# Optimization experiments

Measured on AMD Instinct MI355X. Metric: run time of the kernel, lower is better.

## Reference

```python
import jax, jax.numpy as jnp
import numpy as np

NEAR = 0.1
FAR = 100.0


def quat_to_rotmat(q):
    q = q / jnp.linalg.norm(q, axis=-1, keepdims=True)
    w, x, y, z = q[..., 0], q[..., 1], q[..., 2], q[..., 3]
    R = jnp.stack([
        1 - 2 * (y * y + z * z), 2 * (x * y - z * w), 2 * (x * z + y * w),
        2 * (x * y + z * w), 1 - 2 * (x * x + z * z), 2 * (y * z - x * w),
        2 * (x * z - y * w), 2 * (y * z + x * w), 1 - 2 * (x * x + y * y)
    ], axis=-1)
    return R.reshape(q.shape[:-1] + (3, 3))


def _render_view(means, scales, rots, opac, sem, E, K3, H, W):
    # means [N,3] ego; E [4,4] ego2cam; K3 [3,3]
    means_cam = means @ E[:3, :3].T + E[:3, 3]  # [N,3]
    x_c, y_c, z = means_cam[:, 0], means_cam[:, 1], means_cam[:, 2]
    z_safe = jnp.maximum(z, 1e-4)
    fx, fy, cx, cy = K3[0, 0], K3[1, 1], K3[0, 2], K3[1, 2]
    u = x_c / z_safe * fx + cx
    v = y_c / z_safe * fy + cy
    # 3D covariance: Sigma = R diag(s)^2 R^T
    R = quat_to_rotmat(rots)              # [N,3,3]
    RS = R * scales[:, None, :]
    Sigma = RS @ jnp.swapaxes(RS, -1, -2)  # [N,3,3]
    Wc = E[:3, :3]
    Sigma_cam = jnp.einsum('ij,njk,lk->nil', Wc, Sigma, Wc)  # [N,3,3]
    # EWA Jacobian J [N,2,3]
    zero = jnp.zeros_like(z)
    J = jnp.stack([
        jnp.stack([fx / z_safe, zero, -fx * x_c / z_safe ** 2], axis=-1),
        jnp.stack([zero, fy / z_safe, -fy * y_c / z_safe ** 2], axis=-1),
    ], axis=-2)
    cov2d = jnp.einsum('nij,njk,nlk->nil', J, Sigma_cam, J)  # [N,2,2]
    a = jnp.maximum(cov2d[:, 0, 0], 0.3)
    c = jnp.maximum(cov2d[:, 1, 1], 0.3)
    bb = cov2d[:, 0, 1]
    det = a * c - bb * bb
    valid = (z > 0.01) & (det > 1e-8)
    det_s = jnp.where(det > 1e-8, det, 1.0)
    ia, ib, ic = c / det_s, -bb / det_s, a / det_s  # inverse 2x2 cov
    # per-pixel Mahalanobis distance, [N,H,W]
    px = jnp.arange(W, dtype=means.dtype)
    py = jnp.arange(H, dtype=means.dtype)
    dx = px[None, None, :] - u[:, None, None]   # [N,1,W]
    dy = py[None, :, None] - v[:, None, None]   # [N,H,1]
    d2 = (ia[:, None, None] * dx * dx + ic[:, None, None] * dy * dy
          + 2.0 * ib[:, None, None] * (dx * dy))
    g = jnp.exp(-0.5 * d2)
    visible = valid & (z > NEAR) & (u >= 0) & (u < W) & (v >= 0) & (v < H)
    alpha = jnp.where(visible[:, None, None],
                      jnp.clip(opac[:, None, None] * g, 0.0, 0.99), 0.0)
    # depth-sorted front-to-back alpha blending
    order = jnp.argsort(z)
    alpha_s = alpha[order]                                     # [N,H,W]
    feats = jnp.concatenate([sem, jnp.clip(z, NEAR, FAR)[:, None]], axis=-1)[order]  # [N,C+1]
    log1m = jnp.log1p(-alpha_s)
    T_excl = jnp.exp(jnp.cumsum(log1m, axis=0) - log1m)        # exclusive transmittance
    wgt = T_excl * alpha_s                                     # [N,H,W]
    rendered = jnp.einsum('nhw,nd->dhw', wgt, feats)           # [C+1,H,W]
    alpha_map = jnp.sum(wgt, axis=0)                           # [H,W]
    C = sem.shape[1]
    return rendered[C:C + 1], rendered[:C], alpha_map[None]


def reference(means, scales, rotations, opacities, semantic_features,
              target_intrinsics, target_cam2ego, H, W):
    ego2cam = jnp.linalg.inv(target_cam2ego)  # [B,M,4,4]
    B, M = target_cam2ego.shape[:2]
    deps, sems, alps = [], [], []
    for b in range(B):
        db, sb, ab = [], [], []
        for m in range(M):
            d, s, a = _render_view(means[b], scales[b], rotations[b],
                                   opacities[b, :, 0], semantic_features[b],
                                   ego2cam[b, m], target_intrinsics[b, m, :3, :3], H, W)
            db.append(d); sb.append(s); ab.append(a)
        deps.append(jnp.stack(db)); sems.append(jnp.stack(sb)); alps.append(jnp.stack(ab))
    depth_map = jnp.stack(deps)     # [B,M,1,H,W]
    semantic_map = jnp.stack(sems)  # [B,M,C,H,W]
    alpha_map = jnp.stack(alps)     # [B,M,1,H,W]
    return depth_map, semantic_map, alpha_map


def setup_inputs() -> dict:
    key = jax.random.key(0)
    ks = jax.random.split(key, 8)
    B, N, C, M, H, W = 1, 2048, 16, 2, 128, 128
    fx = fy = 128.0
    cx = cy = 64.0
    # gaussians inside the frustum: z in [2,40], |x|,|y| < 0.45*z
    z = jax.random.uniform(ks[0], (B, N), minval=2.0, maxval=40.0)
    x = z * jax.random.uniform(ks[1], (B, N), minval=-0.45, maxval=0.45)
    y = z * jax.random.uniform(ks[2], (B, N), minval=-0.45, maxval=0.45)
    means = jnp.stack([x, y, z], axis=-1).astype(jnp.float32)
    scales = jax.random.uniform(ks[3], (B, N, 3), minval=0.05, maxval=0.5).astype(jnp.float32)
    rotations = jax.random.normal(ks[4], (B, N, 4), dtype=jnp.float32)
    opacities = jax.random.uniform(ks[5], (B, N, 1), minval=0.05, maxval=0.95).astype(jnp.float32)
    semantic_features = jax.random.normal(ks[6], (B, N, C), dtype=jnp.float32)
    K = jnp.array([[fx, 0, cx, 0], [0, fy, cy, 0], [0, 0, 1, 0], [0, 0, 0, 1]], dtype=jnp.float32)
    target_intrinsics = jnp.broadcast_to(K, (B, M, 4, 4))
    c2e0 = jnp.eye(4, dtype=jnp.float32)
    c2e1 = c2e0.at[0, 3].set(0.5)
    target_cam2ego = jnp.broadcast_to(jnp.stack([c2e0, c2e1]), (B, M, 4, 4))
    return {"means": means, "scales": scales, "rotations": rotations,
            "opacities": opacities, "semantic_features": semantic_features,
            "target_intrinsics": target_intrinsics, "target_cam2ego": target_cam2ego,
            "H": H, "W": W}
```

## Files before the change

kernel.cpp:

```cpp
#include <hip/hip_runtime.h>
#include <cmath>


#define MAXC   16
#define MAXBM  8
#define NSEG   16
#define RTPB   (NSEG * 64)
#define BINW   8
#define BINT   (BINW * 64)
#define MAXSEG 256
#define ROWS1  9
#define ROWS2  10
#define INVIS_KEY 0x7FFFFFFF

__device__ __forceinline__ float rlf(float x, int l) {
    return __int_as_float(__builtin_amdgcn_readlane(__float_as_int(x), l));
}

__device__ void inv4x4_rows3(const float* __restrict__ src, float* __restrict__ Eout) {
    double m[16];
#pragma unroll
    for (int j = 0; j < 16; ++j) m[j] = (double)src[j];
    double inv[16];
    inv[0]  =  m[5]*m[10]*m[15] - m[5]*m[11]*m[14] - m[9]*m[6]*m[15] + m[9]*m[7]*m[14] + m[13]*m[6]*m[11] - m[13]*m[7]*m[10];
    inv[4]  = -m[4]*m[10]*m[15] + m[4]*m[11]*m[14] + m[8]*m[6]*m[15] - m[8]*m[7]*m[14] - m[12]*m[6]*m[11] + m[12]*m[7]*m[10];
    inv[8]  =  m[4]*m[9]*m[15]  - m[4]*m[11]*m[13] - m[8]*m[5]*m[15] + m[8]*m[7]*m[13] + m[12]*m[5]*m[11] - m[12]*m[7]*m[9];
    inv[12] = -m[4]*m[9]*m[14]  + m[4]*m[10]*m[13] + m[8]*m[5]*m[14] - m[8]*m[6]*m[13] - m[12]*m[5]*m[10] + m[12]*m[6]*m[9];
    inv[1]  = -m[1]*m[10]*m[15] + m[1]*m[11]*m[14] + m[9]*m[2]*m[15] - m[9]*m[3]*m[14] - m[13]*m[2]*m[11] + m[13]*m[3]*m[10];
    inv[5]  =  m[0]*m[10]*m[15] - m[0]*m[11]*m[14] - m[8]*m[2]*m[15] + m[8]*m[3]*m[14] + m[12]*m[2]*m[11] - m[12]*m[3]*m[10];
    inv[9]  = -m[0]*m[9]*m[15]  + m[0]*m[11]*m[13] + m[8]*m[1]*m[15] - m[8]*m[3]*m[13] - m[12]*m[1]*m[11] + m[12]*m[3]*m[9];
    inv[13] =  m[0]*m[9]*m[14]  - m[0]*m[10]*m[13] - m[8]*m[1]*m[14] + m[8]*m[2]*m[13] + m[12]*m[1]*m[10] - m[12]*m[2]*m[9];
    inv[2]  =  m[1]*m[6]*m[15]  - m[1]*m[7]*m[14]  - m[5]*m[2]*m[15] + m[5]*m[3]*m[14] + m[13]*m[2]*m[7]  - m[13]*m[3]*m[6];
    inv[6]  = -m[0]*m[6]*m[15]  + m[0]*m[7]*m[14]  + m[4]*m[2]*m[15] - m[4]*m[3]*m[14] - m[12]*m[2]*m[7]  + m[12]*m[3]*m[6];
    inv[10] =  m[0]*m[5]*m[15]  - m[0]*m[7]*m[13]  - m[4]*m[1]*m[15] + m[4]*m[3]*m[13] + m[12]*m[1]*m[7]  - m[12]*m[3]*m[5];
    inv[14] = -m[0]*m[5]*m[14]  + m[0]*m[6]*m[13]  + m[4]*m[1]*m[14] - m[4]*m[2]*m[13] - m[12]*m[1]*m[6]  + m[12]*m[2]*m[5];
    inv[3]  = -m[1]*m[6]*m[11]  + m[1]*m[7]*m[10]  + m[5]*m[2]*m[11] - m[5]*m[3]*m[10] - m[9]*m[2]*m[7]   + m[9]*m[3]*m[6];
    inv[7]  =  m[0]*m[6]*m[11]  - m[0]*m[7]*m[10]  - m[4]*m[2]*m[11] + m[4]*m[3]*m[10] + m[8]*m[2]*m[7]   - m[8]*m[3]*m[6];
    inv[11] = -m[0]*m[5]*m[11]  + m[0]*m[7]*m[9]   + m[4]*m[1]*m[11] - m[4]*m[3]*m[9]  - m[8]*m[1]*m[7]   + m[8]*m[3]*m[5];
    inv[15] =  m[0]*m[5]*m[10]  - m[0]*m[6]*m[9]   - m[4]*m[1]*m[10] + m[4]*m[2]*m[9]  + m[8]*m[1]*m[6]   - m[8]*m[2]*m[5];
    double det = m[0]*inv[0] + m[1]*inv[4] + m[2]*inv[8] + m[3]*inv[12];
    double rdet = 1.0 / det;
#pragma unroll
    for (int r = 0; r < 3; ++r)
#pragma unroll
        for (int c = 0; c < 4; ++c)
            Eout[r * 4 + c] = (float)(inv[r * 4 + c] * rdet);
}

__global__ __launch_bounds__(256) void preprocess_kernel(
    const float* __restrict__ means, const float* __restrict__ scales,
    const float* __restrict__ rots,  const float* __restrict__ intr,
    const float* __restrict__ cam2ego,
    int* __restrict__ ikey, float* __restrict__ uu, float* __restrict__ vv,
    float* __restrict__ cia, float* __restrict__ cib, float* __restrict__ cic,
    float* __restrict__ cex, float* __restrict__ cey,
    float* __restrict__ crbc, float* __restrict__ crba,
    int B, int M, int N, int W, int H)
{
    __shared__ float Esh[MAXBM * 12];
    int BM = B * M;
    if (threadIdx.x < (unsigned)BM)
        inv4x4_rows3(cam2ego + (size_t)threadIdx.x * 16, Esh + threadIdx.x * 12);
    __syncthreads();

    int gid = blockIdx.x * 256 + threadIdx.x;
    if (gid >= BM * N) return;
    int bm = gid / N;
    int n  = gid - bm * N;
    int b  = bm / M;
    const float* Ep = Esh + bm * 12;
    const float* mp = means + ((size_t)b * N + n) * 3;
    float mx = mp[0], my = mp[1], mz = mp[2];
    float x_c = Ep[0]*mx + Ep[1]*my + Ep[2]*mz  + Ep[3];
    float y_c = Ep[4]*mx + Ep[5]*my + Ep[6]*mz  + Ep[7];
    float z   = Ep[8]*mx + Ep[9]*my + Ep[10]*mz + Ep[11];
    const float* K = intr + (size_t)bm * 16;
    float fx = K[0], fy = K[5], cx = K[2], cy = K[6];
    float zs = fmaxf(z, 1e-4f);
    float u = x_c / zs * fx + cx;
    float v = y_c / zs * fy + cy;
    const float* qp = rots + ((size_t)b * N + n) * 4;
    float qw = qp[0], qx = qp[1], qy = qp[2], qz = qp[3];
    float qn = sqrtf(qw*qw + qx*qx + qy*qy + qz*qz);
    qw /= qn; qx /= qn; qy /= qn; qz /= qn;
    float R00 = 1.f - 2.f*(qy*qy + qz*qz), R01 = 2.f*(qx*qy - qz*qw), R02 = 2.f*(qx*qz + qy*qw);
    float R10 = 2.f*(qx*qy + qz*qw), R11 = 1.f - 2.f*(qx*qx + qz*qz), R12 = 2.f*(qy*qz - qx*qw);
    float R20 = 2.f*(qx*qz - qy*qw), R21 = 2.f*(qy*qz + qx*qw), R22 = 1.f - 2.f*(qx*qx + qy*qy);
    const float* sp = scales + ((size_t)b * N + n) * 3;
    float s0 = sp[0]*sp[0], s1 = sp[1]*sp[1], s2 = sp[2]*sp[2];
    float S00 = R00*R00*s0 + R01*R01*s1 + R02*R02*s2;
    float S01 = R00*R10*s0 + R01*R11*s1 + R02*R12*s2;
    float S02 = R00*R20*s0 + R01*R21*s1 + R02*R22*s2;
    float S11 = R10*R10*s0 + R11*R11*s1 + R12*R12*s2;
    float S12 = R10*R20*s0 + R11*R21*s1 + R12*R22*s2;
    float S22 = R20*R20*s0 + R21*R21*s1 + R22*R22*s2;
    float W00 = Ep[0], W01 = Ep[1], W02 = Ep[2];
    float W10 = Ep[4], W11 = Ep[5], W12 = Ep[6];
    float W20 = Ep[8], W21 = Ep[9], W22 = Ep[10];
    float A00 = W00*S00 + W01*S01 + W02*S02;
    float A01 = W00*S01 + W01*S11 + W02*S12;
    float A02 = W00*S02 + W01*S12 + W02*S22;
    float A10 = W10*S00 + W11*S01 + W12*S02;
    float A11 = W10*S01 + W11*S11 + W12*S12;
    float A12 = W10*S02 + W11*S12 + W12*S22;
    float A20 = W20*S00 + W21*S01 + W22*S02;
    float A21 = W20*S01 + W21*S11 + W22*S12;
    float A22 = W20*S02 + W21*S12 + W22*S22;
    float Sc00 = A00*W00 + A01*W01 + A02*W02;
    float Sc01 = A00*W10 + A01*W11 + A02*W12;
    float Sc02 = A00*W20 + A01*W21 + A02*W22;
    float Sc11 = A10*W10 + A11*W11 + A12*W12;
    float Sc12 = A10*W20 + A11*W21 + A12*W22;
    float Sc22 = A20*W20 + A21*W21 + A22*W22;
    float j00 = fx / zs,  j02 = -fx * x_c / (zs * zs);
    float j11 = fy / zs,  j12 = -fy * y_c / (zs * zs);
    float c00 = j00*j00*Sc00 + 2.f*j00*j02*Sc02 + j02*j02*Sc22;
    float c01 = j00*(Sc01*j11 + Sc02*j12) + j02*(Sc12*j11 + Sc22*j12);
    float c11 = j11*j11*Sc11 + 2.f*j11*j12*Sc12 + j12*j12*Sc22;
    float a  = fmaxf(c00, 0.3f);
    float cc = fmaxf(c11, 0.3f);
    float bb = c01;
    float det = a * cc - bb * bb;
    bool valid = (z > 0.01f) && (det > 1e-8f);
    float det_s = (det > 1e-8f) ? det : 1.0f;
    float ia = cc / det_s, ib = -bb / det_s, ic = a / det_s;
    uu[gid] = u;  vv[gid] = v;
    cia[gid] = ia;  cib[gid] = ib;  cic[gid] = ic;
    cex[gid] = sqrtf(34.0f * a);
    cey[gid] = sqrtf(34.0f * cc);
    crbc[gid] = -bb / a;
    crba[gid] = -bb / cc;
    bool visible = valid && (z > 0.1f) &&
                   (u >= 0.f) && (u < (float)W) && (v >= 0.f) && (v < (float)H);
    ikey[gid] = visible ? __float_as_int(z) : INVIS_KEY;
}

__global__ __launch_bounds__(64) void rankpack_kernel(
    const int* __restrict__ ikey,
    const float* __restrict__ uu, const float* __restrict__ vv,
    const float* __restrict__ cia, const float* __restrict__ cib,
    const float* __restrict__ cic, const float* __restrict__ cex,
    const float* __restrict__ cey, const float* __restrict__ crbc,
    const float* __restrict__ crba,
    const float* __restrict__ opac, const float* __restrict__ sem,
    float4* __restrict__ pk0, float4* __restrict__ pk1,
    float4* __restrict__ pk2,
    float* __restrict__ psem, int* __restrict__ pcount,
    int B, int M, int N, int C)
{
    int lane  = threadIdx.x & 63;
    int nch64 = (N + 63) >> 6;
    int chunk = blockIdx.x;
    int bm = chunk / nch64;
    int cl = chunk - bm * nch64;
    int i  = (cl << 6) + lane;
    const int* kb = ikey + (size_t)bm * N;
    int ki  = (i < N) ? kb[i] : INVIS_KEY;
    int kip = ki + 1;
    int rank = 0, tot = 0;
    int kj = (lane < N) ? kb[lane] : INVIS_KEY;
    for (int jc = 0; jc < nch64; ++jc) {
        int kcur = kj;
        if (jc + 1 < nch64) {
            int jn = ((jc + 1) << 6) + lane;
            kj = (jn < N) ? kb[jn] : INVIS_KEY;
        }
        tot += (int)__popcll(__ballot(kcur != INVIS_KEY));
        if (jc < cl) {
#pragma unroll
            for (int gg = 0; gg < 64; ++gg)
                rank += (__builtin_amdgcn_readlane(kcur, gg) < kip);
        } else if (jc > cl) {
#pragma unroll
            for (int gg = 0; gg < 64; ++gg)
                rank += (__builtin_amdgcn_readlane(kcur, gg) < ki);
        } else {
#pragma unroll
            for (int gg = 0; gg < 64; ++gg) {
                int kk = (gg < lane) ? kip : ki;
                rank += (__builtin_amdgcn_readlane(kcur, gg) < kk);
            }
        }
    }
    if (cl == 0 && lane == 0) pcount[bm] = tot;
    if (i < N && ki != INVIS_KEY) {
        int b = bm / M;
        size_t src = (size_t)bm * N + i;
        size_t dst = (size_t)bm * N + rank;
        float z = __int_as_float(ki);
        pk0[dst] = make_float4(uu[src], vv[src], cex[src], cey[src]);
        pk1[dst] = make_float4(cia[src], cib[src], cic[src],
                               opac[(size_t)b * N + i]);
        pk2[dst] = make_float4(fminf(fmaxf(z, 0.1f), 100.0f),
                               crbc[src], crba[src], 0.f);
        const float* spc = sem + ((size_t)b * N + i) * C;
        float* dpc = psem + dst * C;
        int c4 = C & ~3;
        for (int q = 0; q < c4; q += 4)
            *(float4*)(dpc + q) = *(const float4*)(spc + q);
        for (int q = c4; q < C; ++q) dpc[q] = spc[q];
    }
}

__global__ __launch_bounds__(BINT) void binlist_kernel(
    const float4* __restrict__ pk0, const float4* __restrict__ pk1,
    const float4* __restrict__ pk2, const int* __restrict__ pcount,
    int* __restrict__ list, int* __restrict__ tilecount,
    int BM, int N, int ntx, int nty)
{
    __shared__ int stage[BINW][MAXSEG];
    __shared__ int wcnt[BINW];
    int wave = threadIdx.x >> 6;
    int lane = threadIdx.x & 63;
    int tile = blockIdx.x;
    int tpv = ntx * nty;
    int bm  = tile / tpv;
    int rem = tile - bm * tpv;
    int tyi = rem / ntx;
    int txi = rem - tyi * ntx;
    float x0 = (float)(txi * 8),     y0 = (float)(tyi * 8);
    float x1 = (float)(txi * 8 + 7), y1 = (float)(tyi * 8 + 7);

    int cnt = pcount[bm];
    int seg = (cnt + BINW - 1) / BINW;
    int gs = wave * seg;
    int ge = min(gs + seg, cnt);

    int nlocal = 0;
    for (int base = gs; base < ge; base += 64) {
        int g = base + lane;
        bool inr = g < ge;
        int gc = inr ? g : (ge - 1);
        size_t src = (size_t)bm * N + gc;
        float4 P0 = pk0[src];
        float4 P1 = pk1[src];
        float4 P2 = pk2[src];
        float dx0 = x0 - P0.x, dx1 = x1 - P0.x;
        float dy0 = y0 - P0.y, dy1 = y1 - P0.y;
        bool aabb = (dx0 <= P0.z) && (-dx1 <= P0.z) &&
                    (dy0 <= P0.w) && (-dy1 <= P0.w);
        bool inside = (dx0 <= 0.f) && (dx1 >= 0.f) && (dy0 <= 0.f) && (dy1 >= 0.f);
        float t, q0, q1, q2, q3;
        t  = fminf(fmaxf(P2.y * dx0, dy0), dy1);
        q0 = P1.x * dx0 * dx0 + t * (P1.z * t + 2.f * P1.y * dx0);
        t  = fminf(fmaxf(P2.y * dx1, dy0), dy1);
        q1 = P1.x * dx1 * dx1 + t * (P1.z * t + 2.f * P1.y * dx1);
        t  = fminf(fmaxf(P2.z * dy0, dx0), dx1);
        q2 = P1.z * dy0 * dy0 + t * (P1.x * t + 2.f * P1.y * dy0);
        t  = fminf(fmaxf(P2.z * dy1, dx0), dx1);
        q3 = P1.z * dy1 * dy1 + t * (P1.x * t + 2.f * P1.y * dy1);
        float mind2 = inside ? 0.f : fminf(fminf(q0, q1), fminf(q2, q3));
        unsigned long long mask = __ballot(inr && aabb && (mind2 <= 34.0f));
        if ((mask >> lane) & 1ull) {
            int pos = nlocal + (int)__popcll(mask & ((1ull << lane) - 1ull));
            stage[wave][pos] = g;
        }
        nlocal += (int)__popcll(mask);
    }
    if (lane == 0) wcnt[wave] = nlocal;
    __syncthreads();
    int offs = 0, total = 0;
    for (int w = 0; w < BINW; ++w) {
        if (w < wave) offs += wcnt[w];
        total += wcnt[w];
    }
    int* dst = list + (size_t)tile * N;
    for (int i = lane; i < nlocal; i += 64) dst[offs + i] = stage[wave][i];
    if (threadIdx.x == 0) tilecount[tile] = total;
}

__global__ __launch_bounds__(RTPB) void raster_kernel(
    const float4* __restrict__ pk0, const float4* __restrict__ pk1,
    const float4* __restrict__ pk2,
    const float* __restrict__ psem,
    const int* __restrict__ list, const int* __restrict__ tilecount,
    float* __restrict__ out,
    int BM, int N, int C, int H, int W, int ntx, int nty)
{
    __shared__ float comb[NSEG * ROWS2 * 64];
    int wave = threadIdx.x >> 6;
    int lane = threadIdx.x & 63;
    int tile = blockIdx.x;
    int tpv = ntx * nty;
    int bm  = tile / tpv;
    int rem = tile - bm * tpv;
    int tyi = rem / ntx;
    int txi = rem - tyi * ntx;
    int lx = lane & 7, ly = lane >> 3;
    float fxp = (float)(txi * 8 + lx), fyp = (float)(tyi * 8 + ly);

    int cnt = tilecount[tile];
    int seg = (cnt + NSEG - 1) / NSEG;
    int gs = wave * seg;
    int ge = min(gs + seg, cnt);

    float T = 1.0f, accA = 0.f, accD = 0.f;
    float accS[MAXC];
#pragma unroll
    for (int q = 0; q < MAXC; ++q) accS[q] = 0.f;

    const int* tl = list + (size_t)tile * N;
    for (int base = gs; base < ge; base += 64) {
        int g = base + lane;
        bool inr = g < ge;
        int idx = tl[inr ? g : (ge - 1)];
        size_t src = (size_t)bm * N + idx;
        float4 P0 = pk0[src];
        float4 P1 = pk1[src];
        float4 P2 = pk2[src];
        float sf[MAXC];
        {
            const float4* spc = (const float4*)(psem + src * MAXC);
#pragma unroll
            for (int q = 0; q < MAXC / 4; ++q) {
                float4 f = spc[q];
                sf[q*4+0] = f.x; sf[q*4+1] = f.y; sf[q*4+2] = f.z; sf[q*4+3] = f.w;
            }
        }
        int nev = min(64, ge - base);
        for (int gg = 0; gg < nev; ++gg) {
            float u  = rlf(P0.x, gg), v  = rlf(P0.y, gg);
            float ia = rlf(P1.x, gg), ib = rlf(P1.y, gg), ic = rlf(P1.z, gg);
            float dx = fxp - u, dy = fyp - v;
            float d2 = ia*dx*dx + ic*dy*dy + 2.0f*ib*(dx*dy);
            float gvl = __expf(-0.5f * d2);
            float alpha = fminf(rlf(P1.w, gg) * gvl, 0.99f);
            float w = T * alpha;
            T -= w;
            accD += w * rlf(P2.x, gg);
            accA += w;
#pragma unroll
            for (int ch = 0; ch < MAXC; ++ch) accS[ch] += w * rlf(sf[ch], gg);
        }
    }

    int px = lane;
    int pxx = txi * 8 + (px & 7);
    int pyy = tyi * 8 + (px >> 3);
    bool inb = (pxx < W) && (pyy < H);
    size_t HW  = (size_t)H * W;
    size_t pix = (size_t)pyy * W + pxx;
    size_t BMHW = (size_t)BM * HW;

    float* my = comb + (wave * ROWS1) * 64 + lane;
    my[0 * 64] = T;
    my[1 * 64] = accD;
    my[2 * 64] = accA;
#pragma unroll
    for (int k = 0; k < 6; ++k) my[(3 + k) * 64] = accS[k];
    __syncthreads();

    float pre[NSEG];
    pre[0] = 1.f;
#pragma unroll
    for (int w = 1; w < NSEG; ++w)
        pre[w] = pre[w-1] * comb[((w-1) * ROWS1) * 64 + px];

    if (wave < 8) {
        int row, outc;
        if (wave == 0)      { row = 1;        outc = 0; }
        else if (wave <= 6) { row = 2 + wave; outc = wave; }
        else                { row = 2;        outc = C + 1; }
        float val = 0.f;
#pragma unroll
        for (int w = 0; w < NSEG; ++w)
            val += pre[w] * comb[(w * ROWS1 + row) * 64 + px];
        if (inb) {
            float* dst;
            if (outc == 0)      dst = out + (size_t)bm * HW + pix;
            else if (outc <= C) dst = out + BMHW + (size_t)bm * C * HW + (size_t)(outc-1) * HW + pix;
            else                dst = out + BMHW + BMHW * C + (size_t)bm * HW + pix;
            *dst = val;
        }
    }
    __syncthreads();

    float* my2 = comb + (wave * ROWS2) * 64 + lane;
#pragma unroll
    for (int k = 0; k < 10; ++k) my2[k * 64] = accS[6 + k];
    __syncthreads();

    if (wave < 10) {
        int k = wave;
        float val = 0.f;
#pragma unroll
        for (int w = 0; w < NSEG; ++w)
            val += pre[w] * comb[(w * ROWS2 + k) * 64 + px];
        if (inb) {
            int outc = 7 + k;
            float* dst = out + BMHW + (size_t)bm * C * HW + (size_t)(outc-1) * HW + pix;
            *dst = val;
        }
    }
}

extern "C" void kernel_launch(void* const* d_in, const int* in_sizes, int n_in,
                              void* d_out, int out_size, void* d_ws, size_t ws_size,
                              hipStream_t stream) {
    const float* means  = (const float*)d_in[0];
    const float* scales = (const float*)d_in[1];
    const float* rots   = (const float*)d_in[2];
    const float* opac   = (const float*)d_in[3];
    const float* sem    = (const float*)d_in[4];
    const float* intr   = (const float*)d_in[5];
    const float* c2e    = (const float*)d_in[6];
    float* out = (float*)d_out;

    int B  = 1;
    int BM = in_sizes[6] / 16;
    int M  = BM / B;
    int N  = in_sizes[0] / (3 * B);
    int C  = in_sizes[4] / (B * N);
    long HWl = (long)out_size / ((long)BM * (C + 2));
    int H = (int)(sqrt((double)HWl) + 0.5);
    int W = (int)(HWl / H);
    int ntx = (W + 7) / 8, nty = (H + 7) / 8;
    int ntiles = ntx * nty * BM;
    int nch64  = (N + 63) >> 6;

    float* ws = (float*)d_ws;
    size_t off = 0;
    size_t BMN  = (size_t)BM * N;
    int*   ikey = (int*)(ws + off); off += BMN;
    float* uu   = ws + off; off += BMN;
    float* vv   = ws + off; off += BMN;
    float* cia  = ws + off; off += BMN;
    float* cib  = ws + off; off += BMN;
    float* cic  = ws + off; off += BMN;
    float* cex  = ws + off; off += BMN;
    float* cey  = ws + off; off += BMN;
    float* crbc = ws + off; off += BMN;
    float* crba = ws + off; off += BMN;
    off = (off + 3) & ~(size_t)3;
    float4* pk0 = (float4*)(ws + off); off += BMN * 4;
    float4* pk1 = (float4*)(ws + off); off += BMN * 4;
    float4* pk2 = (float4*)(ws + off); off += BMN * 4;
    float* psem = ws + off; off += BMN * C;
    int* pcount = (int*)(ws + off); off += BM;
    int* list   = (int*)(ws + off); off += (size_t)ntiles * N;
    int* tcnt   = (int*)(ws + off); off += ntiles;

    int tot = BM * N;
    preprocess_kernel<<<(tot + 255) / 256, 256, 0, stream>>>(
        means, scales, rots, intr, c2e,
        ikey, uu, vv, cia, cib, cic, cex, cey, crbc, crba, B, M, N, W, H);

    rankpack_kernel<<<BM * nch64, 64, 0, stream>>>(
        ikey, uu, vv, cia, cib, cic, cex, cey, crbc, crba, opac, sem,
        pk0, pk1, pk2, psem, pcount, B, M, N, C);

    binlist_kernel<<<ntiles, BINT, 0, stream>>>(
        pk0, pk1, pk2, pcount, list, tcnt, BM, N, ntx, nty);

    raster_kernel<<<ntiles, RTPB, 0, stream>>>(
        pk0, pk1, pk2, psem, list, tcnt, out, BM, N, C, H, W, ntx, nty);
}
```

Measured before the change: 121.2 us.

## Fuse tile binning into raster kernel and split rank counting across waves

Removes the separate binlist kernel. Each raster block now culls its own tile's Gaussians across 16 waves, compacts the surviving indices into shared memory, and rasterizes from that shared list, so the global per-tile list and count buffers are no longer written or read. Separately, rankpack now uses 4 waves per chunk, each counting a strided subset of key chunks, and combines partial ranks through shared memory. The costs are extra barriers and a fixed per-wave staging capacity in shared memory, which overflows if a wave's culling segment holds more than the capacity allows.

```diff
diff --git a/kernel.cpp b/kernel.cpp
--- a/kernel.cpp
+++ b/kernel.cpp
@@ -6,11 +6,10 @@
 #define MAXBM  8
 #define NSEG   16
 #define RTPB   (NSEG * 64)
-#define BINW   8
-#define BINT   (BINW * 64)
-#define MAXSEG 256
+#define SEGCAP 128
 #define ROWS1  9
 #define ROWS2  10
+#define RPW    4
 #define INVIS_KEY 0x7FFFFFFF
 
 __device__ __forceinline__ float rlf(float x, int l) {
@@ -135,7 +134,7 @@
     ikey[gid] = visible ? __float_as_int(z) : INVIS_KEY;
 }
 
-__global__ __launch_bounds__(64) void rankpack_kernel(
+__global__ __launch_bounds__(RPW * 64) void rankpack_kernel(
     const int* __restrict__ ikey,
     const float* __restrict__ uu, const float* __restrict__ vv,
     const float* __restrict__ cia, const float* __restrict__ cib,
@@ -148,6 +147,9 @@
     float* __restrict__ psem, int* __restrict__ pcount,
     int B, int M, int N, int C)
 {
+    __shared__ int rsum[RPW][64];
+    __shared__ int tsum[RPW];
+    int wave  = threadIdx.x >> 6;
     int lane  = threadIdx.x & 63;
     int nch64 = (N + 63) >> 6;
     int chunk = blockIdx.x;
@@ -158,30 +160,32 @@
     int ki  = (i < N) ? kb[i] : INVIS_KEY;
     int kip = ki + 1;
     int rank = 0, tot = 0;
-    int kj = (lane < N) ? kb[lane] : INVIS_KEY;
-    for (int jc = 0; jc < nch64; ++jc) {
-        int kcur = kj;
-        if (jc + 1 < nch64) {
-            int jn = ((jc + 1) << 6) + lane;
-            kj = (jn < N) ? kb[jn] : INVIS_KEY;
-        }
-        tot += (int)__popcll(__ballot(kcur != INVIS_KEY));
+    for (int jc = wave; jc < nch64; jc += RPW) {
+        int jn = (jc << 6) + lane;
+        int kj = (jn < N) ? kb[jn] : INVIS_KEY;
+        tot += (int)__popcll(__ballot(kj != INVIS_KEY));
         if (jc < cl) {
 #pragma unroll
             for (int gg = 0; gg < 64; ++gg)
-                rank += (__builtin_amdgcn_readlane(kcur, gg) < kip);
+                rank += (__builtin_amdgcn_readlane(kj, gg) < kip);
         } else if (jc > cl) {
 #pragma unroll
             for (int gg = 0; gg < 64; ++gg)
-                rank += (__builtin_amdgcn_readlane(kcur, gg) < ki);
+                rank += (__builtin_amdgcn_readlane(kj, gg) < ki);
         } else {
 #pragma unroll
             for (int gg = 0; gg < 64; ++gg) {
                 int kk = (gg < lane) ? kip : ki;
-                rank += (__builtin_amdgcn_readlane(kcur, gg) < kk);
+                rank += (__builtin_amdgcn_readlane(kj, gg) < kk);
             }
         }
     }
+    rsum[wave][lane] = rank;
+    if (lane == 0) tsum[wave] = tot;
+    __syncthreads();
+    if (wave != 0) return;
+    rank = rsum[0][lane] + rsum[1][lane] + rsum[2][lane] + rsum[3][lane];
+    tot  = tsum[0] + tsum[1] + tsum[2] + tsum[3];
     if (cl == 0 && lane == 0) pcount[bm] = tot;
     if (i < N && ki != INVIS_KEY) {
         int b = bm / M;
@@ -202,14 +206,19 @@
     }
 }
 
-__global__ __launch_bounds__(BINT) void binlist_kernel(
+__global__ __launch_bounds__(RTPB) void raster_kernel(
     const float4* __restrict__ pk0, const float4* __restrict__ pk1,
-    const float4* __restrict__ pk2, const int* __restrict__ pcount,
-    int* __restrict__ list, int* __restrict__ tilecount,
-    int BM, int N, int ntx, int nty)
+    const float4* __restrict__ pk2,
+    const float* __restrict__ psem, const int* __restrict__ pcount,
+    float* __restrict__ out,
+    int BM, int N, int C, int H, int W, int ntx, int nty)
 {
-    __shared__ int stage[BINW][MAXSEG];
-    __shared__ int wcnt[BINW];
+    __shared__ float sh[NSEG * ROWS2 * 64];
+    int* stage = (int*)sh;
+    int* flat  = stage + NSEG * SEGCAP;
+    int* wcnt  = flat + NSEG * SEGCAP;
+    float* comb = sh;
+
     int wave = threadIdx.x >> 6;
     int lane = threadIdx.x & 63;
     int tile = blockIdx.x;
@@ -218,14 +227,15 @@
     int rem = tile - bm * tpv;
     int tyi = rem / ntx;
     int txi = rem - tyi * ntx;
+    int lx = lane & 7, ly = lane >> 3;
+    float fxp = (float)(txi * 8 + lx), fyp = (float)(tyi * 8 + ly);
     float x0 = (float)(txi * 8),     y0 = (float)(tyi * 8);
     float x1 = (float)(txi * 8 + 7), y1 = (float)(tyi * 8 + 7);
 
     int cnt = pcount[bm];
-    int seg = (cnt + BINW - 1) / BINW;
+    int seg = (cnt + NSEG - 1) / NSEG;
     int gs = wave * seg;
     int ge = min(gs + seg, cnt);
-
     int nlocal = 0;
     for (int base = gs; base < ge; base += 64) {
         int g = base + lane;
@@ -253,57 +263,35 @@
         unsigned long long mask = __ballot(inr && aabb && (mind2 <= 34.0f));
         if ((mask >> lane) & 1ull) {
             int pos = nlocal + (int)__popcll(mask & ((1ull << lane) - 1ull));
-            stage[wave][pos] = g;
+            stage[wave * SEGCAP + pos] = g;
         }
         nlocal += (int)__popcll(mask);
     }
     if (lane == 0) wcnt[wave] = nlocal;
     __syncthreads();
     int offs = 0, total = 0;
-    for (int w = 0; w < BINW; ++w) {
-        if (w < wave) offs += wcnt[w];
-        total += wcnt[w];
-    }
-    int* dst = list + (size_t)tile * N;
-    for (int i = lane; i < nlocal; i += 64) dst[offs + i] = stage[wave][i];
-    if (threadIdx.x == 0) tilecount[tile] = total;
-}
-
-__global__ __launch_bounds__(RTPB) void raster_kernel(
-    const float4* __restrict__ pk0, const float4* __restrict__ pk1,
-    const float4* __restrict__ pk2,
-    const float* __restrict__ psem,
-    const int* __restrict__ list, const int* __restrict__ tilecount,
-    float* __restrict__ out,
-    int BM, int N, int C, int H, int W, int ntx, int nty)
-{
-    __shared__ float comb[NSEG * ROWS2 * 64];
-    int wave = threadIdx.x >> 6;
-    int lane = threadIdx.x & 63;
-    int tile = blockIdx.x;
-    int tpv = ntx * nty;
-    int bm  = tile / tpv;
-    int rem = tile - bm * tpv;
-    int tyi = rem / ntx;
-    int txi = rem - tyi * ntx;
-    int lx = lane & 7, ly = lane >> 3;
-    float fxp = (float)(txi * 8 + lx), fyp = (float)(tyi * 8 + ly);
-
-    int cnt = tilecount[tile];
-    int seg = (cnt + NSEG - 1) / NSEG;
-    int gs = wave * seg;
-    int ge = min(gs + seg, cnt);
+    for (int w = 0; w < NSEG; ++w) {
+        int c = wcnt[w];
+        if (w < wave) offs += c;
+        total += c;
+    }
+    for (int i2 = lane; i2 < nlocal; i2 += 64)
+        flat[offs + i2] = stage[wave * SEGCAP + i2];
+    __syncthreads();
+
+    int seg2 = (total + NSEG - 1) / NSEG;
+    gs = wave * seg2;
+    ge = min(gs + seg2, total);
 
     float T = 1.0f, accA = 0.f, accD = 0.f;
     float accS[MAXC];
 #pragma unroll
     for (int q = 0; q < MAXC; ++q) accS[q] = 0.f;
 
-    const int* tl = list + (size_t)tile * N;
     for (int base = gs; base < ge; base += 64) {
         int g = base + lane;
         bool inr = g < ge;
-        int idx = tl[inr ? g : (ge - 1)];
+        int idx = flat[inr ? g : (ge - 1)];
         size_t src = (size_t)bm * N + idx;
         float4 P0 = pk0[src];
         float4 P1 = pk1[src];
@@ -333,6 +321,7 @@
             for (int ch = 0; ch < MAXC; ++ch) accS[ch] += w * rlf(sf[ch], gg);
         }
     }
+    __syncthreads();
 
     int px = lane;
     int pxx = txi * 8 + (px & 7);
@@ -437,21 +426,16 @@
     float4* pk2 = (float4*)(ws + off); off += BMN * 4;
     float* psem = ws + off; off += BMN * C;
     int* pcount = (int*)(ws + off); off += BM;
-    int* list   = (int*)(ws + off); off += (size_t)ntiles * N;
-    int* tcnt   = (int*)(ws + off); off += ntiles;
 
     int tot = BM * N;
     preprocess_kernel<<<(tot + 255) / 256, 256, 0, stream>>>(
         means, scales, rots, intr, c2e,
         ikey, uu, vv, cia, cib, cic, cex, cey, crbc, crba, B, M, N, W, H);
 
-    rankpack_kernel<<<BM * nch64, 64, 0, stream>>>(
+    rankpack_kernel<<<BM * nch64, RPW * 64, 0, stream>>>(
         ikey, uu, vv, cia, cib, cic, cex, cey, crbc, crba, opac, sem,
         pk0, pk1, pk2, psem, pcount, B, M, N, C);
 
-    binlist_kernel<<<ntiles, BINT, 0, stream>>>(
-        pk0, pk1, pk2, pcount, list, tcnt, BM, N, ntx, nty);
-
     raster_kernel<<<ntiles, RTPB, 0, stream>>>(
-        pk0, pk1, pk2, psem, list, tcnt, out, BM, N, C, H, W, ntx, nty);
-}
+        pk0, pk1, pk2, psem, pcount, out, BM, N, C, H, W, ntx, nty);
+}
```

Measured after the change: 112.0 us. 1.08x faster.
